# Optimization experiments

Hardware: AMD Instinct MI355X
Metric: run time of the kernel (lower is better)

Reference implementation:

```python
import jax, jax.numpy as jnp
import numpy as np

E = 1024
H = 16
HD = E // H  # 64


def setup_inputs() -> dict:
    key = jax.random.key(0)
    ks = jax.random.split(key, 5)
    x = jax.random.normal(ks[0], (2, 2048, E), dtype=jnp.float32)
    s = 1.0 / np.sqrt(E)
    W_qkv = jax.random.uniform(ks[1], (E, 3 * E), jnp.float32, -s, s)
    b_qkv = jax.random.uniform(ks[2], (3 * E,), jnp.float32, -s, s)
    W_out = jax.random.uniform(ks[3], (E, E), jnp.float32, -s, s)
    b_out = jax.random.uniform(ks[4], (E,), jnp.float32, -s, s)
    return {"x": x, "W_qkv": W_qkv, "b_qkv": b_qkv, "W_out": W_out, "b_out": b_out}


def reference(x, W_qkv, b_qkv, W_out, b_out):
    B, N, _ = x.shape
    scale = HD ** (-0.5)
    qkv = x @ W_qkv + b_qkv                         # [B, N, 3E]
    qkv = qkv.reshape(B, N, H, 3 * HD)              # torch layout: per-head 3*hd chunk
    qkv = qkv.transpose(0, 2, 1, 3)                 # [B, H, N, 3*hd]
    q, k, v = jnp.split(qkv, 3, axis=-1)            # each [B, H, N, hd]
    attn = jnp.einsum('bhqd,bhkd->bhqk', q, k) * scale
    attn = jax.nn.softmax(attn, axis=-1)            # dropout is identity in eval
    out = jnp.einsum('bhqk,bhkd->bhqd', attn, v)    # [B, H, N, hd]
    out = out.transpose(0, 2, 1, 3).reshape(B, N, E)
    return out @ W_out + b_out
```

## Files before the change

### kernel.cpp

```cpp
#include <hip/hip_runtime.h>


#define SEQ 2048
#define NH  16

typedef __attribute__((ext_vector_type(8))) short short8;
typedef __attribute__((ext_vector_type(4))) short short4v;
typedef __attribute__((ext_vector_type(4))) float floatx4;
typedef __attribute__((ext_vector_type(4))) _Float16 half4;
typedef __attribute__((ext_vector_type(8))) _Float16 half8;
typedef __attribute__((ext_vector_type(2))) _Float16 half2v;
typedef __attribute__((ext_vector_type(2))) __fp16 fp16x2;

#define QSCALE 0.1803368801111204f

__device__ __forceinline__ short f2bf(float f) {
    union { float f; unsigned u; } v; v.f = f;
    unsigned r = v.u + 0x7fffu + ((v.u >> 16) & 1u);
    return (short)(r >> 16);
}

__device__ __forceinline__ float fast_exp2(float x) {
#if __has_builtin(__builtin_amdgcn_exp2f)
    return __builtin_amdgcn_exp2f(x);
#else
    return exp2f(x);
#endif
}

__device__ __forceinline__ half2v cvt_pk(float a, float b) {
#if __has_builtin(__builtin_amdgcn_cvt_pkrtz)
    union { fp16x2 i; half2v o; } u;
    u.i = __builtin_amdgcn_cvt_pkrtz(a, b);
    return u.o;
#else
    half2v r; r.x = (_Float16)a; r.y = (_Float16)b; return r;
#endif
}

#define GLDS16(gp, lp)                                                          \
    __builtin_amdgcn_global_load_lds(                                           \
        (const __attribute__((address_space(1))) unsigned int*)(gp),            \
        (__attribute__((address_space(3))) unsigned int*)(lp), 16, 0, 0)

__global__ __launch_bounds__(256) void prep_kernel(
    const float* __restrict__ x,  short* __restrict__ xb,
    const float* __restrict__ wq, short* __restrict__ wqkvt,
    const float* __restrict__ wo, short* __restrict__ woutt)
{
    const int tid = threadIdx.x;
    const int b = blockIdx.x;
    if (b < 2048) {
        int i = b * 256 + tid;
        const float4* in4 = (const float4*)x + (size_t)i * 2;
        float4 a = in4[0], c = in4[1];
        short8 o = { f2bf(a.x), f2bf(a.y), f2bf(a.z), f2bf(a.w),
                     f2bf(c.x), f2bf(c.y), f2bf(c.z), f2bf(c.w) };
        *((short8*)xb + i) = o;
        return;
    }
    __shared__ float T[64][65];
    const float* in; short* out; int R, C, c0, r0;
    if (b < 2816) {
        int t = b - 2048; in = wq; out = wqkvt; R = 1024; C = 3072;
        c0 = (t % 48) * 64; r0 = (t / 48) * 64;
    } else {
        int t = b - 2816; in = wo; out = woutt; R = 1024; C = 1024;
        c0 = (t & 15) * 64; r0 = (t >> 4) * 64;
    }
#pragma unroll
    for (int it = 0; it < 4; ++it) {
        int r = it * 16 + (tid >> 4), c = (tid & 15) * 4;
        float4 v = *(const float4*)(in + (size_t)(r0 + r) * C + c0 + c);
        T[c+0][r] = v.x; T[c+1][r] = v.y; T[c+2][r] = v.z; T[c+3][r] = v.w;
    }
    __syncthreads();
#pragma unroll
    for (int it = 0; it < 4; ++it) {
        int oc = it * 16 + (tid >> 4), k = (tid & 15) * 4;
        short4v o = { f2bf(T[oc][k]), f2bf(T[oc][k+1]), f2bf(T[oc][k+2]), f2bf(T[oc][k+3]) };
        *(short4v*)(out + (size_t)(c0 + oc) * R + r0 + k) = o;
    }
}

#define GEMM_CORE(A_PTR, B_PTR, LDA, LDB)                                        \
    __shared__ short As[128 * 32];                                               \
    __shared__ short Bs[128 * 32];                                               \
    const int tid  = threadIdx.x;                                                \
    const int lane = tid & 63, w = tid >> 6;                                     \
    const int quad = lane >> 4, l16 = lane & 15;                                 \
    const int wm = w >> 1, wn = w & 1;                                           \
    const int c0 = blockIdx.x * 128, r0 = blockIdx.y * 128;                      \
    floatx4 acc[4][4];                                                           \
    _Pragma("unroll")                                                            \
    for (int i = 0; i < 4; ++i)                                                  \
        _Pragma("unroll")                                                        \
        for (int j = 0; j < 4; ++j) acc[i][j] = (floatx4){0.f, 0.f, 0.f, 0.f};   \
    const int srow = tid >> 2;                                                   \
    const int sgx  = ((tid & 3) ^ ((srow >> 1) & 3)) * 8;                        \
    const short* Ag = (A_PTR) + (size_t)(r0 + srow) * (LDA) + sgx;               \
    const short* Bg = (B_PTR) + (size_t)(c0 + srow) * (LDB) + sgx;               \
    const int fsw = (l16 >> 1) & 3;                                              \
    for (int kk = 0; kk < 1024; kk += 32) {                                      \
        __syncthreads();                                                         \
        GLDS16(Ag + kk,                      As + tid * 8);                      \
        GLDS16(Ag + (size_t)64 * (LDA) + kk, As + 2048 + tid * 8);               \
        GLDS16(Bg + kk,                      Bs + tid * 8);                      \
        GLDS16(Bg + (size_t)64 * (LDB) + kk, Bs + 2048 + tid * 8);               \
        __syncthreads();                                                         \
        short8 af[4], bf[4];                                                     \
        _Pragma("unroll")                                                        \
        for (int mt = 0; mt < 4; ++mt)                                           \
            af[mt] = *(const short8*)&As[(wm * 64 + mt * 16 + l16) * 32 + (quad ^ fsw) * 8]; \
        _Pragma("unroll")                                                        \
        for (int nt = 0; nt < 4; ++nt)                                           \
            bf[nt] = *(const short8*)&Bs[(wn * 64 + nt * 16 + l16) * 32 + (quad ^ fsw) * 8]; \
        _Pragma("unroll")                                                        \
        for (int mt = 0; mt < 4; ++mt)                                           \
            _Pragma("unroll")                                                    \
            for (int nt = 0; nt < 4; ++nt)                                       \
                acc[mt][nt] = __builtin_amdgcn_mfma_f32_16x16x32_bf16(           \
                    af[mt], bf[nt], acc[mt][nt], 0, 0, 0);                       \
    }

__global__ __launch_bounds__(256) void qkv_gemm_kernel(
    const short* __restrict__ wt, const short* __restrict__ xb,
    const float* __restrict__ bias,
    short* __restrict__ qb, short* __restrict__ kb, _Float16* __restrict__ vfb)
{
    GEMM_CORE(wt, xb, 1024, 1024)
#pragma unroll
    for (int mt = 0; mt < 4; ++mt) {
        int oc0 = r0 + wm * 64 + mt * 16 + quad * 4;
        int head = oc0 / 192;
        int t = (oc0 - head * 192) >> 6;
        int d0 = oc0 & 63;
        float4 bv = *(const float4*)(bias + oc0);
#pragma unroll
        for (int nt = 0; nt < 4; ++nt) {
            int tok = c0 + wn * 64 + nt * 16 + l16;
            int bh = (tok >> 11) * NH + head;
            float v0 = acc[mt][nt][0] + bv.x, v1 = acc[mt][nt][1] + bv.y;
            float v2 = acc[mt][nt][2] + bv.z, v3 = acc[mt][nt][3] + bv.w;
            if (t == 2) {
                int n  = tok & (SEQ - 1);
                int h  = nt & 1;
                int qv = l16 >> 2, r = l16 & 3;
                int j  = h * 4 + r;
                size_t vb = (size_t)bh * 131072 + (size_t)(n >> 7) * 8192
                          + (size_t)((n >> 5) & 3) * 2048 + (size_t)d0 * 32 + j;
                _Float16 vv[4] = { (_Float16)v0, (_Float16)v1,
                                   (_Float16)v2, (_Float16)v3 };
#pragma unroll
                for (int jj = 0; jj < 4; ++jj) {
                    int cset = qv ^ (((d0 + jj) >> 1) & 3);
                    vfb[vb + jj * 32 + cset * 8] = vv[jj];
                }
            } else {
                size_t base = ((size_t)bh * SEQ + (tok & (SEQ - 1))) * 64 + d0;
                if (t == 0) {
                    short4v o = { f2bf(v0 * QSCALE), f2bf(v1 * QSCALE),
                                  f2bf(v2 * QSCALE), f2bf(v3 * QSCALE) };
                    *(short4v*)(qb + base) = o;
                } else {
                    short4v o = { f2bf(v0), f2bf(v1), f2bf(v2), f2bf(v3) };
                    *(short4v*)(kb + base) = o;
                }
            }
        }
    }
}

__global__ __launch_bounds__(256) void out_gemm_kernel(
    const short* __restrict__ wt, const short* __restrict__ ab,
    const float* __restrict__ bias, float* __restrict__ out)
{
    __shared__ short As[64 * 32];
    __shared__ short Bs[128 * 32];
    const int tid  = threadIdx.x;
    const int lane = tid & 63, w = tid >> 6;
    const int quad = lane >> 4, l16 = lane & 15;
    const int c0 = blockIdx.x * 128;
    const int r0 = blockIdx.y * 64;
    floatx4 acc[4][2];
#pragma unroll
    for (int i = 0; i < 4; ++i)
#pragma unroll
        for (int j = 0; j < 2; ++j) acc[i][j] = (floatx4){0.f, 0.f, 0.f, 0.f};
    const int srow = tid >> 2;
    const int sgx  = ((tid & 3) ^ ((srow >> 1) & 3)) * 8;
    const short* Ag = wt + (size_t)(r0 + srow) * 1024 + sgx;
    const short* Bg = ab + (size_t)(c0 + srow) * 1024 + sgx;
    const int fsw = (l16 >> 1) & 3;
    for (int kk = 0; kk < 1024; kk += 32) {
        __syncthreads();
        GLDS16(Ag + kk,                   As + tid * 8);
        GLDS16(Bg + kk,                   Bs + tid * 8);
        GLDS16(Bg + (size_t)64 * 1024 + kk, Bs + 2048 + tid * 8);
        __syncthreads();
        short8 af[4], bf[2];
#pragma unroll
        for (int mt = 0; mt < 4; ++mt)
            af[mt] = *(const short8*)&As[(mt * 16 + l16) * 32 + (quad ^ fsw) * 8];
#pragma unroll
        for (int nt = 0; nt < 2; ++nt)
            bf[nt] = *(const short8*)&Bs[(w * 32 + nt * 16 + l16) * 32 + (quad ^ fsw) * 8];
#pragma unroll
        for (int mt = 0; mt < 4; ++mt)
#pragma unroll
            for (int nt = 0; nt < 2; ++nt)
                acc[mt][nt] = __builtin_amdgcn_mfma_f32_16x16x32_bf16(
                    af[mt], bf[nt], acc[mt][nt], 0, 0, 0);
    }
#pragma unroll
    for (int mt = 0; mt < 4; ++mt) {
        int oc0 = r0 + mt * 16 + quad * 4;
        float4 bv = *(const float4*)(bias + oc0);
#pragma unroll
        for (int nt = 0; nt < 2; ++nt) {
            int tok = c0 + w * 32 + nt * 16 + l16;
            float4 o = { acc[mt][nt][0] + bv.x, acc[mt][nt][1] + bv.y,
                         acc[mt][nt][2] + bv.z, acc[mt][nt][3] + bv.w };
            *(float4*)(out + (size_t)tok * 1024 + oc0) = o;
        }
    }
}

__global__ __launch_bounds__(256, 4) void attn_kernel(
    const short* __restrict__ qb, const short* __restrict__ kb,
    const _Float16* __restrict__ vfb, short* __restrict__ ob)
{
    __shared__ short    Ks[128 * 64];
    __shared__ _Float16 Vts[64 * 128];
    __shared__ float    Ls[4][32];
    const int tid  = threadIdx.x;
    const int lane = tid & 63, w = tid >> 6;
    const int quad = lane >> 4, l16 = lane & 15;
    const int qh = w >> 1, kq = w & 1;
    const int lb = blockIdx.x;
    const int bh = (lb & 7) + (((lb >> 3) & 3) << 3);
    const int q0 = (lb >> 5) * 64;

    short8 aq[2][2];
#pragma unroll
    for (int qf = 0; qf < 2; ++qf) {
        const short* qp = qb + ((size_t)bh * SEQ + q0 + qh * 32 + qf * 16 + l16) * 64 + quad * 8;
        aq[qf][0] = *(const short8*)(qp);
        aq[qf][1] = *(const short8*)(qp + 32);
    }

    const int krow = tid >> 3, kg = tid & 7;
    const short* kgp = kb + ((size_t)bh * SEQ + krow) * 64 + (kg ^ (krow & 7)) * 8;
    const short* vgp = (const short*)(vfb + (size_t)bh * 131072) + tid * 8;

    floatx4 o_acc[4][2];
#pragma unroll
    for (int dt = 0; dt < 4; ++dt)
#pragma unroll
        for (int qf = 0; qf < 2; ++qf) o_acc[dt][qf] = (floatx4){0.f, 0.f, 0.f, 0.f};
    float lw[2] = {0.f, 0.f};

    for (int k0 = 0; k0 < SEQ; k0 += 128) {
        __syncthreads();
        const short* kc_p = kgp + (size_t)k0 * 64;
        GLDS16(kc_p,        Ks + tid * 8);
        GLDS16(kc_p + 2048, Ks + 2048 + tid * 8);
        GLDS16(kc_p + 4096, Ks + 4096 + tid * 8);
        GLDS16(kc_p + 6144, Ks + 6144 + tid * 8);
        const short* vc_p = vgp + (size_t)k0 * 64;
        GLDS16(vc_p,        (short*)Vts + tid * 8);
        GLDS16(vc_p + 2048, (short*)Vts + 2048 + tid * 8);
        GLDS16(vc_p + 4096, (short*)Vts + 4096 + tid * 8);
        GLDS16(vc_p + 6144, (short*)Vts + 6144 + tid * 8);
        __syncthreads();

#pragma unroll
        for (int uu = 0; uu < 2; ++uu) {
            const int u = kq * 2 + uu;
            half8 av8[4];
#pragma unroll
            for (int dt = 0; dt < 4; ++dt) {
                union { short8 s; half8 h; } vv;
                vv.s = *(const short8*)((const short*)Vts + u * 2048
                        + (dt * 16 + l16) * 32 + (quad ^ ((l16 >> 1) & 3)) * 8);
                av8[dt] = vv.h;
            }
            floatx4 sacc[2][2];
#pragma unroll
            for (int h = 0; h < 2; ++h) {
                const short* krp = &Ks[(u * 32 + h * 16 + l16) * 64];
                short8 ak0 = *(const short8*)(krp + ((0 + quad) ^ (l16 & 7)) * 8);
                short8 ak1 = *(const short8*)(krp + ((4 + quad) ^ (l16 & 7)) * 8);
                __builtin_amdgcn_s_setprio(1);
#pragma unroll
                for (int qf = 0; qf < 2; ++qf) {
                    floatx4 z = (floatx4){0.f, 0.f, 0.f, 0.f};
                    z = __builtin_amdgcn_mfma_f32_16x16x32_bf16(ak0, aq[qf][0], z, 0, 0, 0);
                    sacc[h][qf] = __builtin_amdgcn_mfma_f32_16x16x32_bf16(ak1, aq[qf][1], z, 0, 0, 0);
                }
                __builtin_amdgcn_s_setprio(0);
            }
            half8 pf8[2];
#pragma unroll
            for (int qf = 0; qf < 2; ++qf) {
                float p0 = fast_exp2(sacc[0][qf][0]);
                float p1 = fast_exp2(sacc[0][qf][1]);
                float p2 = fast_exp2(sacc[0][qf][2]);
                float p3 = fast_exp2(sacc[0][qf][3]);
                float p4 = fast_exp2(sacc[1][qf][0]);
                float p5 = fast_exp2(sacc[1][qf][1]);
                float p6 = fast_exp2(sacc[1][qf][2]);
                float p7 = fast_exp2(sacc[1][qf][3]);
                lw[qf] += ((p0 + p1) + (p2 + p3)) + ((p4 + p5) + (p6 + p7));
                half2v a = cvt_pk(p0, p1), b = cvt_pk(p2, p3);
                half2v c = cvt_pk(p4, p5), d = cvt_pk(p6, p7);
                pf8[qf] = (half8){a.x, a.y, b.x, b.y, c.x, c.y, d.x, d.y};
            }
            __builtin_amdgcn_s_setprio(1);
#pragma unroll
            for (int dt = 0; dt < 4; ++dt)
#pragma unroll
                for (int qf = 0; qf < 2; ++qf)
                    o_acc[dt][qf] = __builtin_amdgcn_mfma_f32_16x16x32_f16(
                        av8[dt], pf8[qf], o_acc[dt][qf], 0, 0, 0);
            __builtin_amdgcn_s_setprio(0);
        }
    }

#pragma unroll
    for (int qf = 0; qf < 2; ++qf) {
        lw[qf] += __shfl_xor(lw[qf], 16);
        lw[qf] += __shfl_xor(lw[qf], 32);
        if (quad == 0) Ls[w][qf * 16 + l16] = lw[qf];
    }

    float* Red = (float*)Ks;
    __syncthreads();
#pragma unroll
    for (int dt = 0; dt < 4; ++dt)
#pragma unroll
        for (int qf = 0; qf < 2; ++qf) {
            int fi = (((qh * 2 + qf) * 4 + dt) * 64 + lane) * 4;
            if (kq == 1) *(floatx4*)&Red[fi] = o_acc[dt][qf];
        }
    __syncthreads();
    if (kq == 0) {
        float inv[2];
#pragma unroll
        for (int qf = 0; qf < 2; ++qf) {
            int qi = qf * 16 + l16;
            inv[qf] = 1.0f / (Ls[qh * 2 + 0][qi] + Ls[qh * 2 + 1][qi]);
        }
        const int b = bh >> 4, h = bh & 15;
#pragma unroll
        for (int dt = 0; dt < 4; ++dt)
#pragma unroll
            for (int qf = 0; qf < 2; ++qf) {
                int fi = (((qh * 2 + qf) * 4 + dt) * 64 + lane) * 4;
                floatx4 o = o_acc[dt][qf] + *(const floatx4*)&Red[fi];
                int tok = b * SEQ + q0 + qh * 32 + qf * 16 + l16;
                short4v o4 = { f2bf(o[0] * inv[qf]), f2bf(o[1] * inv[qf]),
                               f2bf(o[2] * inv[qf]), f2bf(o[3] * inv[qf]) };
                *(short4v*)(ob + (size_t)tok * 1024 + h * 64 + dt * 16 + quad * 4) = o4;
            }
    }
}

extern "C" void kernel_launch(void* const* d_in, const int* in_sizes, int n_in,
                              void* d_out, int out_size, void* d_ws, size_t ws_size,
                              hipStream_t stream) {
    const float* x     = (const float*)d_in[0];
    const float* W_qkv = (const float*)d_in[1];
    const float* b_qkv = (const float*)d_in[2];
    const float* W_out = (const float*)d_in[3];
    const float* b_out = (const float*)d_in[4];
    float* out = (float*)d_out;

    short* xb      = (short*)d_ws;
    short* wqkvt   = xb    + (size_t)4096 * 1024;
    short* woutt   = wqkvt + (size_t)3072 * 1024;
    short* qb      = woutt + (size_t)1024 * 1024;
    short* kb      = qb    + (size_t)32 * SEQ * 64;
    _Float16* vfb  = (_Float16*)(kb + (size_t)32 * SEQ * 64);
    short* ob      = (short*)(vfb + (size_t)32 * 64 * SEQ);

    prep_kernel<<<3072, 256, 0, stream>>>(x, xb, W_qkv, wqkvt, W_out, woutt);
    qkv_gemm_kernel<<<dim3(32, 24), 256, 0, stream>>>(wqkvt, xb, b_qkv, qb, kb, vfb);
    attn_kernel<<<1024, 256, 0, stream>>>(qb, kb, vfb, ob);
    out_gemm_kernel<<<dim3(32, 16), 256, 0, stream>>>(woutt, ob, b_out, out);
}
```

Baseline: 177.6 us.

## Give each attention wave its own query rows instead of splitting keys

The attention kernel now assigns each of the four waves 32 distinct query rows covering all 128 keys per tile, rather than pairing waves over half the keys each. Each block therefore handles 128 queries, so half as many blocks are launched and each K/V tile loaded into shared memory is reused across twice as many queries. This removes the cross-wave reduction of partial outputs and softmax sums through shared memory, along with its extra barriers. In exchange, launch bounds drop to 2 blocks per CU, there are fewer total blocks, and each wave does twice the inner-loop work, which lowers parallelism and occupancy.

```diff
diff --git a/kernel.cpp b/kernel.cpp
--- a/kernel.cpp
+++ b/kernel.cpp
@@ -226,25 +226,23 @@
     }
 }
 
-__global__ __launch_bounds__(256, 4) void attn_kernel(
+__global__ __launch_bounds__(256, 2) void attn_kernel(
     const short* __restrict__ qb, const short* __restrict__ kb,
     const _Float16* __restrict__ vfb, short* __restrict__ ob)
 {
     __shared__ short    Ks[128 * 64];
     __shared__ _Float16 Vts[64 * 128];
-    __shared__ float    Ls[4][32];
     const int tid  = threadIdx.x;
     const int lane = tid & 63, w = tid >> 6;
     const int quad = lane >> 4, l16 = lane & 15;
-    const int qh = w >> 1, kq = w & 1;
     const int lb = blockIdx.x;
     const int bh = (lb & 7) + (((lb >> 3) & 3) << 3);
-    const int q0 = (lb >> 5) * 64;
+    const int q0 = (lb >> 5) * 128;
 
     short8 aq[2][2];
 #pragma unroll
     for (int qf = 0; qf < 2; ++qf) {
-        const short* qp = qb + ((size_t)bh * SEQ + q0 + qh * 32 + qf * 16 + l16) * 64 + quad * 8;
+        const short* qp = qb + ((size_t)bh * SEQ + q0 + w * 32 + qf * 16 + l16) * 64 + quad * 8;
         aq[qf][0] = *(const short8*)(qp);
         aq[qf][1] = *(const short8*)(qp + 32);
     }
@@ -275,8 +273,7 @@
         __syncthreads();
 
 #pragma unroll
-        for (int uu = 0; uu < 2; ++uu) {
-            const int u = kq * 2 + uu;
+        for (int u = 0; u < 4; ++u) {
             half8 av8[4];
 #pragma unroll
             for (int dt = 0; dt < 4; ++dt) {
@@ -327,43 +324,25 @@
         }
     }
 
+    float inv[2];
 #pragma unroll
     for (int qf = 0; qf < 2; ++qf) {
         lw[qf] += __shfl_xor(lw[qf], 16);
         lw[qf] += __shfl_xor(lw[qf], 32);
-        if (quad == 0) Ls[w][qf * 16 + l16] = lw[qf];
-    }
-
-    float* Red = (float*)Ks;
-    __syncthreads();
+        inv[qf] = 1.0f / lw[qf];
+    }
+
+    const int b = bh >> 4, h = bh & 15;
 #pragma unroll
     for (int dt = 0; dt < 4; ++dt)
 #pragma unroll
         for (int qf = 0; qf < 2; ++qf) {
-            int fi = (((qh * 2 + qf) * 4 + dt) * 64 + lane) * 4;
-            if (kq == 1) *(floatx4*)&Red[fi] = o_acc[dt][qf];
+            int tok = b * SEQ + q0 + w * 32 + qf * 16 + l16;
+            floatx4 o = o_acc[dt][qf];
+            short4v o4 = { f2bf(o[0] * inv[qf]), f2bf(o[1] * inv[qf]),
+                           f2bf(o[2] * inv[qf]), f2bf(o[3] * inv[qf]) };
+            *(short4v*)(ob + (size_t)tok * 1024 + h * 64 + dt * 16 + quad * 4) = o4;
         }
-    __syncthreads();
-    if (kq == 0) {
-        float inv[2];
-#pragma unroll
-        for (int qf = 0; qf < 2; ++qf) {
-            int qi = qf * 16 + l16;
-            inv[qf] = 1.0f / (Ls[qh * 2 + 0][qi] + Ls[qh * 2 + 1][qi]);
-        }
-        const int b = bh >> 4, h = bh & 15;
-#pragma unroll
-        for (int dt = 0; dt < 4; ++dt)
-#pragma unroll
-            for (int qf = 0; qf < 2; ++qf) {
-                int fi = (((qh * 2 + qf) * 4 + dt) * 64 + lane) * 4;
-                floatx4 o = o_acc[dt][qf] + *(const floatx4*)&Red[fi];
-                int tok = b * SEQ + q0 + qh * 32 + qf * 16 + l16;
-                short4v o4 = { f2bf(o[0] * inv[qf]), f2bf(o[1] * inv[qf]),
-                               f2bf(o[2] * inv[qf]), f2bf(o[3] * inv[qf]) };
-                *(short4v*)(ob + (size_t)tok * 1024 + h * 64 + dt * 16 + quad * 4) = o4;
-            }
-    }
 }
 
 extern "C" void kernel_launch(void* const* d_in, const int* in_sizes, int n_in,
@@ -386,6 +365,6 @@
 
     prep_kernel<<<3072, 256, 0, stream>>>(x, xb, W_qkv, wqkvt, W_out, woutt);
     qkv_gemm_kernel<<<dim3(32, 24), 256, 0, stream>>>(wqkvt, xb, b_qkv, qb, kb, vfb);
-    attn_kernel<<<1024, 256, 0, stream>>>(qb, kb, vfb, ob);
+    attn_kernel<<<512, 256, 0, stream>>>(qb, kb, vfb, ob);
     out_gemm_kernel<<<dim3(32, 16), 256, 0, stream>>>(woutt, ob, b_out, out);
 }
```

Measured after the change: 174.3 us, median of 2. No clear change (-1.9%).
